# Kernel optimization log

Hardware: AMD Instinct MI355X
Metric: run time of the kernel (lower is better)

The kernel has to match this reference:

```python
import jax, jax.numpy as jnp
import numpy as np

TAU = 0.07          # temperature
NUM_CLASSES = 1000  # label vocabulary size (used for bincount length)


def setup_inputs() -> dict:
    key = jax.random.key(0)
    kq, kk, ky = jax.random.split(key, 3)
    N, K, D = 8192, 8, 512
    q = jax.random.normal(kq, (N, D), dtype=jnp.float32)
    q = q / jnp.linalg.norm(q, axis=1, keepdims=True)          # L2-normalized anchors
    k = jax.random.normal(kk, (N, K, D), dtype=jnp.float32)
    k = k / jnp.linalg.norm(k, axis=2, keepdims=True)          # L2-normalized positives
    y = jax.random.randint(ky, (N,), 0, NUM_CLASSES, dtype=jnp.int32)
    return {"q": q, "k": k, "y": y}


def reference(q, k, y):
    # q: [N, D] anchors, k: [N, K, D] external positives, y: [N] labels
    N, K, D = k.shape
    neg_inf = jnp.float32(-jnp.inf)

    # similarities to external positives and within-batch, scaled by temperature
    k_sims = jnp.einsum('nd,nkd->nk', q, k) / TAU            # [N, K]
    batch_sims = jnp.matmul(q, q.T) / TAU                    # [N, N]

    same = y[:, None] == y[None, :]                          # [N, N] label equality
    eye = jnp.eye(N, dtype=bool)
    same_class_mask = same & ~eye                            # in-batch positives (excl. self)
    same_class_counts = same_class_mask.sum(axis=1) + K      # [N]

    # faithful to torch: multiply by mask then masked_fill(x == 0, -inf)
    batch_pos = batch_sims * same_class_mask
    batch_pos = jnp.where(batch_pos == 0, neg_inf, batch_pos)
    pos_sims = jnp.concatenate([k_sims, batch_pos], axis=1)  # [N, K+N]
    num = jax.scipy.special.logsumexp(pos_sims, axis=1)      # [N]

    y_counts = jnp.bincount(y, length=NUM_CLASSES)           # [C]
    neg_sims = batch_sims * (~same)
    neg_sims = jnp.where(neg_sims == 0, neg_inf, neg_sims)
    # class-frequency-weighted denominator (as in the original, no max-shift)
    den = jnp.log(jnp.sum(jnp.exp(neg_sims) / y_counts[y][None, :].astype(q.dtype), axis=1))

    loss = -(num - den) / same_class_counts.astype(q.dtype)
    return loss.mean()
```

## Files before the change

kernel.cpp:

```cpp
#include <hip/hip_runtime.h>
#include <hip/hip_fp8.h>
#include <stdint.h>

constexpr int N    = 8192;
constexpr int D    = 512;
constexpr int KEXT = 8;
constexpr int NCLS = 1000;
#define TAU_INV  14.285714285714285714f
#define SQRT_TI  3.7796447300922722f

constexpr int BM = 128, BN = 128;
constexpr int NB   = N / BM;
constexpr int NBLK = NB * (NB + 1) / 2;

typedef long   long2_t __attribute__((ext_vector_type(2)));
typedef float  f32x4   __attribute__((ext_vector_type(4)));

__device__ __forceinline__ uint32_t pack4_e4m3(float a, float b, float c, float d) {
    __hip_fp8_e4m3 A(a), B(b), C(c), D(d);
    return (uint32_t)A.__x | ((uint32_t)B.__x << 8) |
           ((uint32_t)C.__x << 16) | ((uint32_t)D.__x << 24);
}

__global__ void prep_k(const float* __restrict__ q, const int* __restrict__ y,
                       uint32_t* __restrict__ qf8, int* __restrict__ counts,
                       float* __restrict__ invc, float* __restrict__ pos,
                       float* __restrict__ neg) {
    const int b = blockIdx.x, tid = threadIdx.x;
    if (b == 0) {
        __shared__ int h[NCLS];
        for (int i = tid; i < NCLS; i += 256) h[i] = 0;
        __syncthreads();
        for (int i = tid; i < N; i += 256) atomicAdd(&h[y[i]], 1);
        __syncthreads();
        for (int i = tid; i < NCLS; i += 256) {
            int c = h[i];
            counts[i] = c;
            invc[i]   = 1.0f / (float)c;
        }
        return;
    }
    const int gid = (b - 1) * 256 + tid;
    const int row = gid >> 5;
    const int c   = gid & 31;
    const int ks2 = c >> 2, quad = c & 3;
    const float* src = q + (size_t)row * D + ks2 * 64 + quad * 8;
    float4 v0 = *reinterpret_cast<const float4*>(src);
    float4 v1 = *reinterpret_cast<const float4*>(src + 4);
    float4 v2 = *reinterpret_cast<const float4*>(src + 32);
    float4 v3 = *reinterpret_cast<const float4*>(src + 36);
    uint4 o;
    o.x = pack4_e4m3(v0.x * SQRT_TI, v0.y * SQRT_TI, v0.z * SQRT_TI, v0.w * SQRT_TI);
    o.y = pack4_e4m3(v1.x * SQRT_TI, v1.y * SQRT_TI, v1.z * SQRT_TI, v1.w * SQRT_TI);
    o.z = pack4_e4m3(v2.x * SQRT_TI, v2.y * SQRT_TI, v2.z * SQRT_TI, v2.w * SQRT_TI);
    o.w = pack4_e4m3(v3.x * SQRT_TI, v3.y * SQRT_TI, v3.z * SQRT_TI, v3.w * SQRT_TI);
    const int t = row >> 4, l15 = row & 15;
    reinterpret_cast<uint4*>(qf8)[(size_t)t * 512 + ks2 * 64 + quad * 16 + l15] = o;
    if (gid < N) { pos[gid] = 0.f; neg[gid] = 0.f; }
}

__global__ __launch_bounds__(256, 3) void gemm_k(
        const uint32_t* __restrict__ qf8,
        const int* __restrict__ y,
        const float* __restrict__ invc,
        float* __restrict__ pos_sum,
        float* __restrict__ neg_sum) {
    __shared__ int   yis[BM];
    __shared__ int   yjs[BN];
    __shared__ float icsA[BM];
    __shared__ float icsB[BN];

    const int tid  = threadIdx.x;
    const int wave = tid >> 6;
    const int lane = tid & 63;
    const int quad = lane >> 4;
    const int l15  = lane & 15;

    const int t = blockIdx.x;
    int bi = (int)(((float)(2 * NB + 1) -
                    sqrtf((float)((2 * NB + 1) * (2 * NB + 1)) - 8.0f * (float)t)) * 0.5f);
    if (bi < 0) bi = 0;
    if (bi > NB - 1) bi = NB - 1;
    while ((bi + 1) * NB - ((bi + 1) * bi >> 1) <= t) ++bi;
    while (bi * NB - (bi * (bi - 1) >> 1) > t) --bi;
    const int bj = bi + (t - (bi * NB - (bi * (bi - 1) >> 1)));
    const int ibase = bi * BM, jbase = bj * BN;

    if (tid < BM) {
        int yi = y[ibase + tid];
        int yj = y[jbase + tid];
        yis[tid] = yi;  icsA[tid] = invc[yi];
        yjs[tid] = yj;  icsB[tid] = invc[yj];
    }
    __syncthreads();

    const int wr = (wave >> 1) * 64;
    const int wc = (wave & 1) * 64;

    f32x4 acc[4][4];
#pragma unroll
    for (int a = 0; a < 4; a++)
#pragma unroll
        for (int b = 0; b < 4; b++) acc[a][b] = (f32x4)0.0f;

    const long2_t* fb = reinterpret_cast<const long2_t*>(qf8);
    const long2_t* pA[4];
    const long2_t* pB[4];
#pragma unroll
    for (int m = 0; m < 4; m++) {
        pA[m] = fb + (size_t)(bi * 8 + (wr >> 4) + m) * 512 + lane;
        pB[m] = fb + (size_t)(bj * 8 + (wc >> 4) + m) * 512 + lane;
    }

    long2_t af[2][4], bf[2][4];
#pragma unroll
    for (int m = 0; m < 4; m++) { af[0][m] = pA[m][0]; bf[0][m] = pB[m][0]; }

#pragma unroll
    for (int ks2 = 0; ks2 < 8; ks2++) {
        const int cur = ks2 & 1, nxt = cur ^ 1;
        if (ks2 < 7) {
#pragma unroll
            for (int m = 0; m < 4; m++) {
                af[nxt][m] = pA[m][(ks2 + 1) * 64];
                bf[nxt][m] = pB[m][(ks2 + 1) * 64];
            }
        }
#pragma unroll
        for (int mi = 0; mi < 4; mi++)
#pragma unroll
            for (int mj = 0; mj < 4; mj++)
                acc[mi][mj] = __builtin_amdgcn_mfma_f32_16x16x32_fp8_fp8(
                    af[cur][mi].x, bf[cur][mj].x, acc[mi][mj], 0, 0, 0);
#pragma unroll
        for (int mi = 0; mi < 4; mi++)
#pragma unroll
            for (int mj = 0; mj < 4; mj++)
                acc[mi][mj] = __builtin_amdgcn_mfma_f32_16x16x32_fp8_fp8(
                    af[cur][mi].y, bf[cur][mj].y, acc[mi][mj], 0, 0, 0);
    }

    int   yjv[4];
    float icj[4];
#pragma unroll
    for (int mj = 0; mj < 4; mj++) {
        int jl = wc + mj * 16 + l15;
        yjv[mj] = yjs[jl];
        icj[mj] = icsB[jl];
    }

    if (bi == bj) {
#pragma unroll
        for (int mi = 0; mi < 4; mi++) {
#pragma unroll
            for (int r = 0; r < 4; r++) {
                const int il   = wr + mi * 16 + quad * 4 + r;
                const int irow = ibase + il;
                const int yi   = yis[il];
                float posp = 0.f, negp = 0.f;
#pragma unroll
                for (int mj = 0; mj < 4; mj++) {
                    const int jcol = jbase + wc + mj * 16 + l15;
                    float a    = acc[mi][mj][r];
                    float e    = __expf(a);
                    bool  nz   = (a != 0.0f);
                    bool  same = (yi == yjv[mj]);
                    posp += (same && (irow != jcol) && nz) ? e : 0.0f;
                    negp += (!same && nz) ? e * icj[mj] : 0.0f;
                }
#pragma unroll
                for (int off = 1; off < 16; off <<= 1) {
                    posp += __shfl_xor(posp, off);
                    negp += __shfl_xor(negp, off);
                }
                if (l15 == 0) {
                    atomicAdd(&pos_sum[irow], posp);
                    atomicAdd(&neg_sum[irow], negp);
                }
            }
        }
    } else {
        float cp[4] = {0.f, 0.f, 0.f, 0.f};
        float cn[4] = {0.f, 0.f, 0.f, 0.f};
#pragma unroll
        for (int mi = 0; mi < 4; mi++) {
#pragma unroll
            for (int r = 0; r < 4; r++) {
                const int il   = wr + mi * 16 + quad * 4 + r;
                const int irow = ibase + il;
                const int yi   = yis[il];
                const float ici = icsA[il];
                float posp = 0.f, negp = 0.f;
#pragma unroll
                for (int mj = 0; mj < 4; mj++) {
                    float a    = acc[mi][mj][r];
                    float e    = __expf(a);
                    bool  nz   = (a != 0.0f);
                    bool  same = (yi == yjv[mj]);
                    float pe   = (same && nz) ? e : 0.0f;
                    posp   += pe;
                    cp[mj] += pe;
                    negp   += (!same && nz) ? e * icj[mj] : 0.0f;
                    cn[mj] += (!same && nz) ? e * ici : 0.0f;
                }
#pragma unroll
                for (int off = 1; off < 16; off <<= 1) {
                    posp += __shfl_xor(posp, off);
                    negp += __shfl_xor(negp, off);
                }
                if (l15 == 0) {
                    atomicAdd(&pos_sum[irow], posp);
                    atomicAdd(&neg_sum[irow], negp);
                }
            }
        }
#pragma unroll
        for (int mj = 0; mj < 4; mj++) {
            float a = cp[mj], b = cn[mj];
            a += __shfl_xor(a, 16); a += __shfl_xor(a, 32);
            b += __shfl_xor(b, 16); b += __shfl_xor(b, 32);
            if (quad == 0) {
                const int jcol = jbase + wc + mj * 16 + l15;
                atomicAdd(&pos_sum[jcol], a);
                atomicAdd(&neg_sum[jcol], b);
            }
        }
    }
}

__global__ void finalize_k(const float* __restrict__ q, const float* __restrict__ kmat,
                           const int* __restrict__ y, const int* __restrict__ counts,
                           const float* __restrict__ pos_sum, const float* __restrict__ neg_sum,
                           float* __restrict__ loss) {
    const int wave = threadIdx.x >> 6, lane = threadIdx.x & 63;
    const int i = blockIdx.x * 4 + wave;

    const float4* q4 = reinterpret_cast<const float4*>(q) + (size_t)i * 128;
    const float4* k4 = reinterpret_cast<const float4*>(kmat) + (size_t)i * KEXT * 128;
    float4 qa = q4[lane], qb = q4[lane + 64];

    float esum = 0.f;
    for (int kk = 0; kk < KEXT; kk++) {
        float4 ka = k4[(size_t)kk * 128 + lane];
        float4 kb = k4[(size_t)kk * 128 + lane + 64];
        float p = qa.x * ka.x;
        p = fmaf(qa.y, ka.y, p); p = fmaf(qa.z, ka.z, p); p = fmaf(qa.w, ka.w, p);
        p = fmaf(qb.x, kb.x, p); p = fmaf(qb.y, kb.y, p);
        p = fmaf(qb.z, kb.z, p); p = fmaf(qb.w, kb.w, p);
#pragma unroll
        for (int off = 1; off < 64; off <<= 1) p += __shfl_xor(p, off);
        esum += __expf(p * TAU_INV);
    }
    if (lane == 0) {
        float num = logf(esum + pos_sum[i]);
        float den = logf(neg_sum[i]);
        float cnt = (float)(counts[y[i]] - 1 + KEXT);
        loss[i] = -(num - den) / cnt;
    }
}

__global__ void reduce_k(const float* __restrict__ loss, float* __restrict__ out) {
    __shared__ float part[16];
    int tid = threadIdx.x;
    float s = 0.f;
    for (int i = tid; i < N; i += 1024) s += loss[i];
#pragma unroll
    for (int off = 1; off < 64; off <<= 1) s += __shfl_xor(s, off);
    if ((tid & 63) == 0) part[tid >> 6] = s;
    __syncthreads();
    if (tid < 16) {
        float v = part[tid];
#pragma unroll
        for (int off = 1; off < 16; off <<= 1) v += __shfl_xor(v, off);
        if (tid == 0) out[0] = v / (float)N;
    }
}

extern "C" void kernel_launch(void* const* d_in, const int* in_sizes, int n_in,
                              void* d_out, int out_size, void* d_ws, size_t ws_size,
                              hipStream_t stream) {
    const float* q    = (const float*)d_in[0];
    const float* kmat = (const float*)d_in[1];
    const int*   y    = (const int*)d_in[2];
    float* out = (float*)d_out;

    char* ws = (char*)d_ws;
    uint32_t* qf8  = (uint32_t*)ws;
    int*   counts  = (int*)  (ws + 4194304);
    float* invc    = (float*)(ws + 4198400);
    float* pos     = (float*)(ws + 4202496);
    float* neg     = (float*)(ws + 4235264);
    float* loss    = (float*)(ws + 4268032);

    prep_k    <<<1 + (N * 32) / 256, 256, 0, stream>>>(q, y, qf8, counts, invc, pos, neg);
    gemm_k    <<<NBLK, 256, 0, stream>>>(qf8, y, invc, pos, neg);
    finalize_k<<<N / 4, 256, 0, stream>>>(q, kmat, y, counts, pos, neg, loss);
    reduce_k  <<<1, 1024, 0, stream>>>(loss, out);
}
```

Measured before the change: 354.2 us.

## Compute full similarity matrix per row block with LDS-resident A tile

Replaces the upper-triangular symmetric tiling with full row-block strips: each block keeps its 128-row fp8 A tile in LDS via global_load_lds and sweeps 1024 columns, accumulating per-row sums in registers. Per-row reductions go through LDS, leaving one atomic per row per block, and the column-side accumulation and most global atomics are gone. In exchange, the GEMM and exp work double because symmetry is no longer exploited, and occupancy bounds drop to 2.

After: 329.9 us. 6.8% less time.

```diff
diff --git a/kernel.cpp b/kernel.cpp
--- a/kernel.cpp
+++ b/kernel.cpp
@@ -9,12 +9,11 @@
 #define TAU_INV  14.285714285714285714f
 #define SQRT_TI  3.7796447300922722f
 
-constexpr int BM = 128, BN = 128;
-constexpr int NB   = N / BM;
-constexpr int NBLK = NB * (NB + 1) / 2;
-
 typedef long   long2_t __attribute__((ext_vector_type(2)));
 typedef float  f32x4   __attribute__((ext_vector_type(4)));
+
+typedef __attribute__((address_space(1))) void gvoid;
+typedef __attribute__((address_space(3))) void lvoid;
 
 __device__ __forceinline__ uint32_t pack4_e4m3(float a, float b, float c, float d) {
     __hip_fp8_e4m3 A(a), B(b), C(c), D(d);
@@ -24,7 +23,7 @@
 
 __global__ void prep_k(const float* __restrict__ q, const int* __restrict__ y,
                        uint32_t* __restrict__ qf8, int* __restrict__ counts,
-                       float* __restrict__ invc, float* __restrict__ pos,
+                       float* __restrict__ invy, float* __restrict__ pos,
                        float* __restrict__ neg) {
     const int b = blockIdx.x, tid = threadIdx.x;
     if (b == 0) {
@@ -33,11 +32,8 @@
         __syncthreads();
         for (int i = tid; i < N; i += 256) atomicAdd(&h[y[i]], 1);
         __syncthreads();
-        for (int i = tid; i < NCLS; i += 256) {
-            int c = h[i];
-            counts[i] = c;
-            invc[i]   = 1.0f / (float)c;
-        }
+        for (int i = tid; i < NCLS; i += 256) counts[i] = h[i];
+        for (int i = tid; i < N; i += 256) invy[i] = 1.0f / (float)h[y[i]];
         return;
     }
     const int gid = (b - 1) * 256 + tid;
@@ -59,16 +55,16 @@
     if (gid < N) { pos[gid] = 0.f; neg[gid] = 0.f; }
 }
 
-__global__ __launch_bounds__(256, 3) void gemm_k(
+__global__ __launch_bounds__(256, 2) void gemm_k(
         const uint32_t* __restrict__ qf8,
         const int* __restrict__ y,
-        const float* __restrict__ invc,
+        const float* __restrict__ invy,
         float* __restrict__ pos_sum,
         float* __restrict__ neg_sum) {
-    __shared__ int   yis[BM];
-    __shared__ int   yjs[BN];
-    __shared__ float icsA[BM];
-    __shared__ float icsB[BN];
+    __shared__ long2_t Asl[4096];
+    __shared__ int   yR[128];
+    __shared__ float redP[2][128];
+    __shared__ float redN[2][128];
 
     const int tid  = threadIdx.x;
     const int wave = tid >> 6;
@@ -76,155 +72,143 @@
     const int quad = lane >> 4;
     const int l15  = lane & 15;
 
-    const int t = blockIdx.x;
-    int bi = (int)(((float)(2 * NB + 1) -
-                    sqrtf((float)((2 * NB + 1) * (2 * NB + 1)) - 8.0f * (float)t)) * 0.5f);
-    if (bi < 0) bi = 0;
-    if (bi > NB - 1) bi = NB - 1;
-    while ((bi + 1) * NB - ((bi + 1) * bi >> 1) <= t) ++bi;
-    while (bi * NB - (bi * (bi - 1) >> 1) > t) --bi;
-    const int bj = bi + (t - (bi * NB - (bi * (bi - 1) >> 1)));
-    const int ibase = bi * BM, jbase = bj * BN;
-
-    if (tid < BM) {
-        int yi = y[ibase + tid];
-        int yj = y[jbase + tid];
-        yis[tid] = yi;  icsA[tid] = invc[yi];
-        yjs[tid] = yj;  icsB[tid] = invc[yj];
-    }
+    const int ib     = blockIdx.x >> 3;
+    const int jchunk = blockIdx.x & 7;
+    const int ibase  = ib * 128;
+
+    {
+        const uint32_t* src = qf8 + (size_t)ib * 16384;
+#pragma unroll
+        for (int it = 0; it < 16; it++) {
+            const int idx = it * 256 + tid;
+            __builtin_amdgcn_global_load_lds((gvoid*)(src + idx * 4),
+                                             (lvoid*)(Asl + idx), 16, 0, 0);
+        }
+    }
+    if (tid < 128) yR[tid] = y[ibase + tid];
     __syncthreads();
 
     const int wr = (wave >> 1) * 64;
     const int wc = (wave & 1) * 64;
-
-    f32x4 acc[4][4];
-#pragma unroll
-    for (int a = 0; a < 4; a++)
-#pragma unroll
-        for (int b = 0; b < 4; b++) acc[a][b] = (f32x4)0.0f;
+    const int half = wave & 1;
+
+    int yi[16];
+#pragma unroll
+    for (int mi = 0; mi < 4; mi++)
+#pragma unroll
+        for (int r = 0; r < 4; r++)
+            yi[mi * 4 + r] = yR[wr + mi * 16 + quad * 4 + r];
+
+    float posp[16], negp[16];
+#pragma unroll
+    for (int e = 0; e < 16; e++) { posp[e] = 0.f; negp[e] = 0.f; }
 
     const long2_t* fb = reinterpret_cast<const long2_t*>(qf8);
-    const long2_t* pA[4];
     const long2_t* pB[4];
 #pragma unroll
-    for (int m = 0; m < 4; m++) {
-        pA[m] = fb + (size_t)(bi * 8 + (wr >> 4) + m) * 512 + lane;
-        pB[m] = fb + (size_t)(bj * 8 + (wc >> 4) + m) * 512 + lane;
-    }
-
-    long2_t af[2][4], bf[2][4];
-#pragma unroll
-    for (int m = 0; m < 4; m++) { af[0][m] = pA[m][0]; bf[0][m] = pB[m][0]; }
-
-#pragma unroll
-    for (int ks2 = 0; ks2 < 8; ks2++) {
-        const int cur = ks2 & 1, nxt = cur ^ 1;
-        if (ks2 < 7) {
-#pragma unroll
-            for (int m = 0; m < 4; m++) {
-                af[nxt][m] = pA[m][(ks2 + 1) * 64];
-                bf[nxt][m] = pB[m][(ks2 + 1) * 64];
-            }
-        }
-#pragma unroll
-        for (int mi = 0; mi < 4; mi++)
-#pragma unroll
-            for (int mj = 0; mj < 4; mj++)
-                acc[mi][mj] = __builtin_amdgcn_mfma_f32_16x16x32_fp8_fp8(
-                    af[cur][mi].x, bf[cur][mj].x, acc[mi][mj], 0, 0, 0);
-#pragma unroll
-        for (int mi = 0; mi < 4; mi++)
-#pragma unroll
-            for (int mj = 0; mj < 4; mj++)
-                acc[mi][mj] = __builtin_amdgcn_mfma_f32_16x16x32_fp8_fp8(
-                    af[cur][mi].y, bf[cur][mj].y, acc[mi][mj], 0, 0, 0);
-    }
-
-    int   yjv[4];
-    float icj[4];
-#pragma unroll
-    for (int mj = 0; mj < 4; mj++) {
-        int jl = wc + mj * 16 + l15;
-        yjv[mj] = yjs[jl];
-        icj[mj] = icsB[jl];
-    }
-
-    if (bi == bj) {
+    for (int m = 0; m < 4; m++)
+        pB[m] = fb + (size_t)(jchunk * 64 + (wc >> 4) + m) * 512 + lane;
+
+    const int tA = wr >> 4;
+
+    for (int jt = 0; jt < 8; jt++) {
+        const int j0 = jchunk * 1024 + jt * 128;
+
+        int   yjv[4];
+        float icj[4];
+#pragma unroll
+        for (int mj = 0; mj < 4; mj++) {
+            int jc = j0 + wc + mj * 16 + l15;
+            yjv[mj] = y[jc];
+            icj[mj] = invy[jc];
+        }
+
+        f32x4 acc[4][4];
+#pragma unroll
+        for (int a = 0; a < 4; a++)
+#pragma unroll
+            for (int c = 0; c < 4; c++) acc[a][c] = (f32x4)0.0f;
+
+        long2_t af[2][4], bf[2][4];
+#pragma unroll
+        for (int m = 0; m < 4; m++) {
+            af[0][m] = Asl[(tA + m) * 512 + lane];
+            bf[0][m] = pB[m][0];
+        }
+#pragma unroll
+        for (int ks2 = 0; ks2 < 8; ks2++) {
+            const int cur = ks2 & 1, nxt = cur ^ 1;
+            if (ks2 < 7) {
+#pragma unroll
+                for (int m = 0; m < 4; m++) {
+                    af[nxt][m] = Asl[(tA + m) * 512 + (ks2 + 1) * 64 + lane];
+                    bf[nxt][m] = pB[m][(ks2 + 1) * 64];
+                }
+            }
+#pragma unroll
+            for (int mi = 0; mi < 4; mi++)
+#pragma unroll
+                for (int mj = 0; mj < 4; mj++)
+                    acc[mi][mj] = __builtin_amdgcn_mfma_f32_16x16x32_fp8_fp8(
+                        af[cur][mi].x, bf[cur][mj].x, acc[mi][mj], 0, 0, 0);
+#pragma unroll
+            for (int mi = 0; mi < 4; mi++)
+#pragma unroll
+                for (int mj = 0; mj < 4; mj++)
+                    acc[mi][mj] = __builtin_amdgcn_mfma_f32_16x16x32_fp8_fp8(
+                        af[cur][mi].y, bf[cur][mj].y, acc[mi][mj], 0, 0, 0);
+        }
+#pragma unroll
+        for (int m = 0; m < 4; m++) pB[m] += 4096;
+
 #pragma unroll
         for (int mi = 0; mi < 4; mi++) {
 #pragma unroll
             for (int r = 0; r < 4; r++) {
-                const int il   = wr + mi * 16 + quad * 4 + r;
-                const int irow = ibase + il;
-                const int yi   = yis[il];
-                float posp = 0.f, negp = 0.f;
+                const int e    = mi * 4 + r;
+                const int irow = ibase + wr + mi * 16 + quad * 4 + r;
+                const int myi  = yi[e];
+                float ps = 0.f, ns = 0.f;
 #pragma unroll
                 for (int mj = 0; mj < 4; mj++) {
-                    const int jcol = jbase + wc + mj * 16 + l15;
+                    const int jcol = j0 + wc + mj * 16 + l15;
                     float a    = acc[mi][mj][r];
-                    float e    = __expf(a);
+                    float ex   = __expf(a);
                     bool  nz   = (a != 0.0f);
-                    bool  same = (yi == yjv[mj]);
-                    posp += (same && (irow != jcol) && nz) ? e : 0.0f;
-                    negp += (!same && nz) ? e * icj[mj] : 0.0f;
+                    bool  same = (myi == yjv[mj]);
+                    ps += (same && (irow != jcol) && nz) ? ex : 0.0f;
+                    ns += (!same && nz) ? ex * icj[mj] : 0.0f;
                 }
-#pragma unroll
-                for (int off = 1; off < 16; off <<= 1) {
-                    posp += __shfl_xor(posp, off);
-                    negp += __shfl_xor(negp, off);
-                }
-                if (l15 == 0) {
-                    atomicAdd(&pos_sum[irow], posp);
-                    atomicAdd(&neg_sum[irow], negp);
-                }
-            }
-        }
-    } else {
-        float cp[4] = {0.f, 0.f, 0.f, 0.f};
-        float cn[4] = {0.f, 0.f, 0.f, 0.f};
-#pragma unroll
-        for (int mi = 0; mi < 4; mi++) {
-#pragma unroll
-            for (int r = 0; r < 4; r++) {
-                const int il   = wr + mi * 16 + quad * 4 + r;
-                const int irow = ibase + il;
-                const int yi   = yis[il];
-                const float ici = icsA[il];
-                float posp = 0.f, negp = 0.f;
-#pragma unroll
-                for (int mj = 0; mj < 4; mj++) {
-                    float a    = acc[mi][mj][r];
-                    float e    = __expf(a);
-                    bool  nz   = (a != 0.0f);
-                    bool  same = (yi == yjv[mj]);
-                    float pe   = (same && nz) ? e : 0.0f;
-                    posp   += pe;
-                    cp[mj] += pe;
-                    negp   += (!same && nz) ? e * icj[mj] : 0.0f;
-                    cn[mj] += (!same && nz) ? e * ici : 0.0f;
-                }
-#pragma unroll
-                for (int off = 1; off < 16; off <<= 1) {
-                    posp += __shfl_xor(posp, off);
-                    negp += __shfl_xor(negp, off);
-                }
-                if (l15 == 0) {
-                    atomicAdd(&pos_sum[irow], posp);
-                    atomicAdd(&neg_sum[irow], negp);
-                }
-            }
-        }
-#pragma unroll
-        for (int mj = 0; mj < 4; mj++) {
-            float a = cp[mj], b = cn[mj];
-            a += __shfl_xor(a, 16); a += __shfl_xor(a, 32);
-            b += __shfl_xor(b, 16); b += __shfl_xor(b, 32);
-            if (quad == 0) {
-                const int jcol = jbase + wc + mj * 16 + l15;
-                atomicAdd(&pos_sum[jcol], a);
-                atomicAdd(&neg_sum[jcol], b);
-            }
-        }
+                posp[e] += ps;
+                negp[e] += ns;
+            }
+        }
+    }
+
+#pragma unroll
+    for (int mi = 0; mi < 4; mi++) {
+#pragma unroll
+        for (int r = 0; r < 4; r++) {
+            const int e = mi * 4 + r;
+            float ps = posp[e], ns = negp[e];
+#pragma unroll
+            for (int off = 1; off < 16; off <<= 1) {
+                ps += __shfl_xor(ps, off);
+                ns += __shfl_xor(ns, off);
+            }
+            if (l15 == 0) {
+                const int il = wr + mi * 16 + quad * 4 + r;
+                redP[half][il] = ps;
+                redN[half][il] = ns;
+            }
+        }
+    }
+    __syncthreads();
+    if (tid < 128) {
+        atomicAdd(&pos_sum[ibase + tid], redP[0][tid] + redP[1][tid]);
+    } else if (tid < 256) {
+        const int il = tid - 128;
+        atomicAdd(&neg_sum[ibase + il], redN[0][il] + redN[1][il]);
     }
 }
 
@@ -287,13 +271,13 @@
     char* ws = (char*)d_ws;
     uint32_t* qf8  = (uint32_t*)ws;
     int*   counts  = (int*)  (ws + 4194304);
-    float* invc    = (float*)(ws + 4198400);
-    float* pos     = (float*)(ws + 4202496);
-    float* neg     = (float*)(ws + 4235264);
-    float* loss    = (float*)(ws + 4268032);
-
-    prep_k    <<<1 + (N * 32) / 256, 256, 0, stream>>>(q, y, qf8, counts, invc, pos, neg);
-    gemm_k    <<<NBLK, 256, 0, stream>>>(qf8, y, invc, pos, neg);
+    float* invy    = (float*)(ws + 4198400);
+    float* pos     = (float*)(ws + 4231168);
+    float* neg     = (float*)(ws + 4263936);
+    float* loss    = (float*)(ws + 4296704);
+
+    prep_k    <<<1 + (N * 32) / 256, 256, 0, stream>>>(q, y, qf8, counts, invy, pos, neg);
+    gemm_k    <<<512, 256, 0, stream>>>(qf8, y, invy, pos, neg);
     finalize_k<<<N / 4, 256, 0, stream>>>(q, kmat, y, counts, pos, neg, loss);
     reduce_k  <<<1, 1024, 0, stream>>>(loss, out);
 }
```
